# Kernel optimization log

Hardware: AMD Instinct MI355X
Metric: run time of the kernel (lower is better)

## Reference

```python
import jax, jax.numpy as jnp
import numpy as np

SCALE = 0.1
TEMP = 1.0
LN_EPS = 1e-6
NORM_EPS = 1e-12  # torch F.normalize eps

def setup_inputs() -> dict:
    key = jax.random.key(0)
    k1, = jax.random.split(key, 1)
    x = jax.random.normal(k1, (8192, 512), dtype=jnp.float32)
    gamma = jnp.ones((512,), dtype=jnp.float32)
    beta = jnp.zeros((512,), dtype=jnp.float32)
    return {"x": x, "gamma": gamma, "beta": beta}

def reference(x, gamma, beta):
    # L2-normalize rows (torch F.normalize semantics: x / max(||x||, eps))
    norm = jnp.maximum(jnp.linalg.norm(x, axis=1, keepdims=True), NORM_EPS)
    xn = x / norm                                   # [N, d]
    sim = (xn @ xn.T) / TEMP                        # [N, N]
    # dual_norm: row softmax + column softmax
    sim = jax.nn.softmax(sim, axis=1) + jax.nn.softmax(sim, axis=0)
    x_neg = sim @ x                                 # [N, d]
    y = x - SCALE * x_neg
    # LayerNorm over last dim, eps=1e-6
    mean = jnp.mean(y, axis=-1, keepdims=True)
    var = jnp.mean(jnp.square(y - mean), axis=-1, keepdims=True)
    out = (y - mean) * jax.lax.rsqrt(var + LN_EPS) * gamma + beta
    return out
```

## Files before the change

kernel.cpp:

```cpp
#include <hip/hip_runtime.h>
#include <math.h>

#define NN 8192
#define DD 512

constexpr float SCALE_C = 0.1f;
constexpr float LN_EPS_C = 1e-6f;
constexpr float NORM_EPS_C = 1e-12f;
constexpr float CBIG = 32768.0f;
constexpr float INV_CBIG = 1.0f / 32768.0f;

typedef __attribute__((ext_vector_type(8))) short bf16x8;
typedef __attribute__((ext_vector_type(4))) float f32x4;

#define MFMA16(a, b, c) __builtin_amdgcn_mfma_f32_16x16x32_bf16((a), (b), (c), 0, 0, 0)
#define MFMA8(a, b, c)                                                        \
  __builtin_amdgcn_mfma_f32_16x16x32_fp8_fp8((long)(a), (long)(b), (c), 0, 0, 0)

#define GLL16(g, l)                                                        \
  __builtin_amdgcn_global_load_lds(                                        \
      (const __attribute__((address_space(1))) unsigned int*)(g),          \
      (__attribute__((address_space(3))) unsigned int*)(l), 16, 0, 0)

#define WAITV4() asm volatile("s_waitcnt vmcnt(4)" ::: "memory")
#define WAITV0() asm volatile("s_waitcnt vmcnt(0)" ::: "memory")
#define WAITLGKM0() asm volatile("s_waitcnt lgkmcnt(0)" ::: "memory")
#define FENCE() asm volatile("" ::: "memory")
#define BAR() __builtin_amdgcn_s_barrier()

__device__ inline unsigned short f2bf(float f) {
  unsigned int u = __builtin_bit_cast(unsigned int, f);
  unsigned int r = (u + 0x7FFFu + ((u >> 16) & 1u)) >> 16;
  return (unsigned short)r;
}

__device__ inline unsigned int f2fp8n(float f) {
  unsigned int a = __builtin_bit_cast(unsigned int, f);
  unsigned int r = a + 0x7FFFFu + ((a >> 20) & 1u);
  return (r >> 20) - 960u;
}

__device__ inline unsigned int f2fp8(float f) {
  unsigned int u = __builtin_bit_cast(unsigned int, f);
  unsigned int s = (u >> 24) & 0x80u;
  unsigned int a = u & 0x7fffffffu;
  if (a >= 0x3C800000u) {
    unsigned int r = a + 0x7FFFFu + ((a >> 20) & 1u);
    return s | ((r >> 20) - 960u);
  }
  float af = __builtin_bit_cast(float, a);
  return s | (unsigned int)(int)rintf(af * 512.0f);
}

__device__ inline float fp82f(unsigned int b) {
  return __builtin_bit_cast(float, (b + 960u) << 20);
}

__global__ __launch_bounds__(256) void k_prep2(const float* __restrict__ x,
                                               unsigned short* __restrict__ xnb,
                                               unsigned char* __restrict__ xT8) {
  __shared__ unsigned int T8w[16][130];
  const int j0 = blockIdx.x * 16;
  const int t = threadIdx.x;
  const int tr = t >> 4, tc = t & 15;
  const int row = j0 + tr;
  const float* xr = x + (size_t)row * DD;
  float4 v[8];
  float ss = 0.f;
#pragma unroll
  for (int k = 0; k < 8; ++k) {
    v[k] = *(const float4*)(xr + tc * 4 + k * 64);
    ss += v[k].x * v[k].x + v[k].y * v[k].y + v[k].z * v[k].z + v[k].w * v[k].w;
  }
#pragma unroll
  for (int off = 1; off < 16; off <<= 1) ss += __shfl_xor(ss, off);
  const float rn = 1.0f / fmaxf(sqrtf(ss), NORM_EPS_C);
#pragma unroll
  for (int k = 0; k < 8; ++k) {
    ushort4 o;
    o.x = f2bf(v[k].x * rn);
    o.y = f2bf(v[k].y * rn);
    o.z = f2bf(v[k].z * rn);
    o.w = f2bf(v[k].w * rn);
    *(ushort4*)(xnb + (size_t)row * DD + tc * 4 + k * 64) = o;
    T8w[tr][tc + k * 16] = f2fp8(v[k].x) | (f2fp8(v[k].y) << 8) |
                           (f2fp8(v[k].z) << 16) | (f2fp8(v[k].w) << 24);
  }
  __syncthreads();
#pragma unroll
  for (int q = 0; q < 2; ++q) {
    const int d = t + q * 256;
    const unsigned char* col = (const unsigned char*)&T8w[0][0] + d;
    unsigned int wds[4];
#pragma unroll
    for (int p = 0; p < 4; ++p)
      wds[p] = (unsigned int)col[(p * 4 + 0) * 520] |
               ((unsigned int)col[(p * 4 + 1) * 520] << 8) |
               ((unsigned int)col[(p * 4 + 2) * 520] << 16) |
               ((unsigned int)col[(p * 4 + 3) * 520] << 24);
    *(uint4*)&xT8[(size_t)d * NN + j0] = make_uint4(wds[0], wds[1], wds[2], wds[3]);
  }
}

__global__ __launch_bounds__(256, 4) void k_rowsumE(const unsigned short* __restrict__ xnb,
                                                    float* __restrict__ lpart,
                                                    unsigned char* __restrict__ E8) {
  __shared__ __align__(16) unsigned char POOL[32768];
  __shared__ float red[4][64];
  __shared__ float red2[4][64];

  int b = blockIdx.x, bi = 0;
  while (b >= 64 - bi) { b -= 64 - bi; ++bi; }
  const int bj = bi + b;
  const int i0 = bi * 128, j0 = bj * 128;
  const int diag = (bi == bj);

  const int t = threadIdx.x;
  const int w = t >> 6, l = t & 63;
  const int lr = l & 15, lg = l >> 4;
  const int wr = w >> 1, wc = w & 1;
  const int r0 = w * 16 + (l >> 2);
  const int clog = (l & 3) ^ ((r0 >> 1) & 3);
  const unsigned short* gA = xnb + (size_t)(i0 + r0) * DD + clog * 8;
  const unsigned short* gB = xnb + (size_t)(j0 + r0) * DD + clog * 8;

#define RS_STAGE(s, koff)                                                        \
  do {                                                                           \
    GLL16(gA + (koff), (unsigned short*)(POOL + (s) * 16384) + w * 512);         \
    GLL16(gA + (size_t)64 * DD + (koff),                                         \
          (unsigned short*)(POOL + (s) * 16384 + 4096) + w * 512);               \
    GLL16(gB + (koff), (unsigned short*)(POOL + (s) * 16384 + 8192) + w * 512);  \
    GLL16(gB + (size_t)64 * DD + (koff),                                         \
          (unsigned short*)(POOL + (s) * 16384 + 12288) + w * 512);              \
  } while (0)

  RS_STAGE(0, 0);
  RS_STAGE(1, 32);

  f32x4 acc[4][4] = {};
  for (int ks = 0; ks < 16; ++ks) {
    if (ks + 1 < 16) { WAITV4(); } else { WAITV0(); }
    BAR(); FENCE();
    const char* AS = (const char*)(POOL + (ks & 1) * 16384);
    const char* BS = AS + 8192;
    bf16x8 af[4], bv[4];
#pragma unroll
    for (int fm = 0; fm < 4; ++fm) {
      const int row = wr * 64 + fm * 16 + lr;
      af[fm] = *(const bf16x8*)(AS + row * 64 + ((lg ^ ((row >> 1) & 3)) << 4));
    }
#pragma unroll
    for (int fn = 0; fn < 4; ++fn) {
      const int row = wc * 64 + fn * 16 + lr;
      bv[fn] = *(const bf16x8*)(BS + row * 64 + ((lg ^ ((row >> 1) & 3)) << 4));
    }
    WAITLGKM0();
    BAR(); FENCE();
    if (ks + 2 < 16) RS_STAGE(ks & 1, (size_t)(ks + 2) * 32);
#pragma unroll
    for (int fm = 0; fm < 4; ++fm)
#pragma unroll
      for (int fn = 0; fn < 4; ++fn)
        acc[fm][fn] = MFMA16(af[fm], bv[fn], acc[fm][fn]);
  }

  unsigned int ebw[4][4];
  float rsum[4][4] = {};
  float csum[4] = {};
#pragma unroll
  for (int fm = 0; fm < 4; ++fm)
#pragma unroll
    for (int fn = 0; fn < 4; ++fn) {
      unsigned int pw = 0;
#pragma unroll
      for (int rr = 0; rr < 4; ++rr) {
        float e = __expf(acc[fm][fn][rr]);
        rsum[fm][rr] += e;
        csum[fn] += e;
        pw |= f2fp8n(e) << (8 * rr);
      }
      ebw[fm][fn] = pw;
    }

#pragma unroll
  for (int fm = 0; fm < 4; ++fm)
#pragma unroll
    for (int rr = 0; rr < 4; ++rr) {
      float s = rsum[fm][rr];
#pragma unroll
      for (int off = 1; off < 16; off <<= 1) s += __shfl_xor(s, off);
      if (lr == 0) red[w][fm * 16 + lg * 4 + rr] = s;
    }
  if (!diag) {
#pragma unroll
    for (int fn = 0; fn < 4; ++fn) {
      float cs = csum[fn];
      cs += __shfl_xor(cs, 16);
      cs += __shfl_xor(cs, 32);
      if (lg == 0) red2[w][fn * 16 + lr] = cs;
    }
  }

  unsigned char(*Et2)[144] = (unsigned char(*)[144])POOL;
#pragma unroll
  for (int fm = 0; fm < 4; ++fm)
#pragma unroll
    for (int fn = 0; fn < 4; ++fn)
      *(unsigned int*)&Et2[wc * 64 + fn * 16 + lr][wr * 64 + fm * 16 + lg * 4] =
          ebw[fm][fn];
  __syncthreads();
  {
    unsigned char* dst2 = E8 + ((size_t)(bj * 64 + bi) << 14);
#pragma unroll
    for (int q = 0; q < 4; ++q) {
      const int f = t + q * 256;
      *(uint4*)(dst2 + f * 16) = *(const uint4*)&Et2[f >> 3][(f & 7) * 16];
    }
  }
  if (t < 128) {
    const int wrx = t >> 6, idx = t & 63;
    lpart[(size_t)bj * NN + i0 + t] = red[2 * wrx][idx] + red[2 * wrx + 1][idx];
  } else if (!diag) {
    const int c = t - 128;
    const int wcx = c >> 6, idx = c & 63;
    lpart[(size_t)bi * NN + j0 + c] = red2[wcx][idx] + red2[2 + wcx][idx];
  }
}

__global__ __launch_bounds__(256) void k_recip(const float* __restrict__ lpart,
                                               float* __restrict__ rl) {
  const int i = blockIdx.x * 256 + threadIdx.x;
  float s = 0.f;
  for (int c = 0; c < 64; ++c) s += lpart[(size_t)c * NN + i];
  rl[i] = CBIG / s;
}

__global__ __launch_bounds__(256) void k_scale2(unsigned char* __restrict__ P,
                                                const float* __restrict__ rl) {
  __shared__ unsigned int T32[128][35];
  int b = blockIdx.x, ti = 0;
  while (b >= 64 - ti) { b -= 64 - ti; ++ti; }
  const int tj = ti + b;
  const int i0 = ti * 128, j0 = tj * 128;
  const int t = threadIdx.x;
  unsigned char* tileC = P + ((size_t)(tj * 64 + ti) << 14);

#pragma unroll
  for (int q = 0; q < 4; ++q) {
    const int f = t + q * 256;
    const int r = f >> 3;
    const int c0 = (f & 7) * 16;
    uint4 v = *(const uint4*)(tileC + f * 16);
    const float rlr = rl[j0 + r];
    float rlc[16];
#pragma unroll
    for (int p = 0; p < 4; ++p) {
      float4 r4 = *(const float4*)(rl + i0 + c0 + p * 4);
      rlc[p * 4 + 0] = r4.x; rlc[p * 4 + 1] = r4.y;
      rlc[p * 4 + 2] = r4.z; rlc[p * 4 + 3] = r4.w;
    }
    unsigned int wsrc[4] = {v.x, v.y, v.z, v.w};
    unsigned int wdst[4];
#pragma unroll
    for (int p = 0; p < 4; ++p) {
      unsigned int in = wsrc[p], out = 0;
#pragma unroll
      for (int k = 0; k < 4; ++k) {
        float e = fp82f((in >> (8 * k)) & 0xffu);
        out |= f2fp8n(e * (rlr + rlc[p * 4 + k])) << (8 * k);
      }
      wdst[p] = out;
      T32[r][(c0 >> 2) + p] = out;
    }
    *(uint4*)(tileC + f * 16) = make_uint4(wdst[0], wdst[1], wdst[2], wdst[3]);
  }
  if (ti == tj) return;
  __syncthreads();

  unsigned char* tileT = P + ((size_t)(ti * 64 + tj) << 14);
  {
    const int rg = t >> 3;
    const int cc = t & 7;
    const int c2 = cc * 16;
    unsigned int o[4][4];
#pragma unroll
    for (int k4 = 0; k4 < 4; ++k4) {
      unsigned int a0 = T32[c2 + k4 * 4 + 0][rg];
      unsigned int a1 = T32[c2 + k4 * 4 + 1][rg];
      unsigned int a2 = T32[c2 + k4 * 4 + 2][rg];
      unsigned int a3 = T32[c2 + k4 * 4 + 3][rg];
      unsigned int b0 = (a0 & 0x00FF00FFu) | ((a1 << 8) & 0xFF00FF00u);
      unsigned int b1 = ((a0 >> 8) & 0x00FF00FFu) | (a1 & 0xFF00FF00u);
      unsigned int b2 = (a2 & 0x00FF00FFu) | ((a3 << 8) & 0xFF00FF00u);
      unsigned int b3 = ((a2 >> 8) & 0x00FF00FFu) | (a3 & 0xFF00FF00u);
      o[0][k4] = (b0 & 0x0000FFFFu) | (b2 << 16);
      o[1][k4] = (b1 & 0x0000FFFFu) | (b3 << 16);
      o[2][k4] = (b0 >> 16) | (b2 & 0xFFFF0000u);
      o[3][k4] = (b1 >> 16) | (b3 & 0xFFFF0000u);
    }
#pragma unroll
    for (int i = 0; i < 4; ++i)
      *(uint4*)(tileT + (size_t)(rg * 4 + i) * 128 + c2) =
          make_uint4(o[i][0], o[i][1], o[i][2], o[i][3]);
  }
}

__global__ __launch_bounds__(256, 4) void k_pv3(const unsigned char* __restrict__ P8,
                                                const unsigned char* __restrict__ xT8,
                                                unsigned short* __restrict__ parts) {
  __shared__ __align__(16) unsigned char POOL[34816];
  const int i0 = blockIdx.x * 128;
  const int n0 = blockIdx.y * 128;
  const int z = blockIdx.z;
  const int t = threadIdx.x;
  const int w = t >> 6, l = t & 63;
  const int lr = l & 15, lg = l >> 4;
  const int wr = w >> 1, wc = w & 1;
  const int r0 = w * 16 + (l >> 2);
  const int clog = (l & 3) ^ ((r0 >> 1) & 3);
  const unsigned char* Abase = P8 + ((size_t)((i0 >> 7) * 64 + z * 16) << 14) +
                               r0 * 128 + clog * 16;
  const unsigned char* gB = xT8 + (size_t)(n0 + r0) * NN + z * 2048 + clog * 16;

#define PV_STAGE(s, koff)                                                      \
  do {                                                                         \
    const unsigned char* a_ = Abase + (((koff) >> 7) << 14) + ((koff) & 127);  \
    GLL16(a_, POOL + (s) * 8192 + w * 1024);                                   \
    GLL16(a_ + 8192, POOL + (s) * 8192 + 4096 + w * 1024);                     \
    GLL16(gB + (koff), POOL + 16384 + (s) * 8192 + w * 1024);                  \
    GLL16(gB + (size_t)64 * NN + (koff),                                       \
          POOL + 16384 + (s) * 8192 + 4096 + w * 1024);                        \
  } while (0)

  PV_STAGE(0, 0);
  PV_STAGE(1, 64);

  f32x4 acc[4][4] = {};
  for (int ks = 0; ks < 32; ++ks) {
    if (ks + 1 < 32) { WAITV4(); } else { WAITV0(); }
    BAR(); FENCE();
    const char* AS = (const char*)(POOL + (ks & 1) * 8192);
    const char* BS = (const char*)(POOL + 16384 + (ks & 1) * 8192);
    unsigned long long af[4][2], bv[4][2];
#pragma unroll
    for (int fm = 0; fm < 4; ++fm) {
      const int row = wr * 64 + fm * 16 + lr;
      const int swz = (row >> 1) & 3;
#pragma unroll
      for (int kk = 0; kk < 2; ++kk) {
        int off = row * 64 + (((kk * 2 + (lg >> 1)) ^ swz) << 4) + ((lg & 1) << 3);
        af[fm][kk] = *(const unsigned long long*)(AS + off);
      }
    }
#pragma unroll
    for (int fn = 0; fn < 4; ++fn) {
      const int row = wc * 64 + fn * 16 + lr;
      const int swz = (row >> 1) & 3;
#pragma unroll
      for (int kk = 0; kk < 2; ++kk) {
        int off = row * 64 + (((kk * 2 + (lg >> 1)) ^ swz) << 4) + ((lg & 1) << 3);
        bv[fn][kk] = *(const unsigned long long*)(BS + off);
      }
    }
    WAITLGKM0();
    BAR(); FENCE();
    if (ks + 2 < 32) PV_STAGE(ks & 1, (ks + 2) * 64);
#pragma unroll
    for (int kk = 0; kk < 2; ++kk)
#pragma unroll
      for (int fm = 0; fm < 4; ++fm)
#pragma unroll
        for (int fn = 0; fn < 4; ++fn)
          acc[fm][fn] = MFMA8(af[fm][kk], bv[fn][kk], acc[fm][fn]);
  }

  BAR(); FENCE();
  unsigned short* Pt = (unsigned short*)POOL;
#pragma unroll
  for (int fm = 0; fm < 4; ++fm)
#pragma unroll
    for (int fn = 0; fn < 4; ++fn) {
      const int col = wc * 64 + fn * 16 + lr;
#pragma unroll
      for (int rr = 0; rr < 4; ++rr) {
        const int row = wr * 64 + fm * 16 + lg * 4 + rr;
        Pt[row * 136 + col] = f2bf(acc[fm][fn][rr] * INV_CBIG);
      }
    }
  __syncthreads();
  {
    unsigned short* dst = parts + (size_t)z * NN * DD + (size_t)i0 * DD + n0;
#pragma unroll
    for (int q = 0; q < 8; ++q) {
      const int f = t + q * 256;
      const int row = f >> 4, ch = f & 15;
      *(uint4*)(dst + (size_t)row * DD + ch * 8) =
          *(const uint4*)&Pt[row * 136 + ch * 8];
    }
  }
}

__global__ __launch_bounds__(128) void k_ln(const float* __restrict__ x,
                                            float* __restrict__ out,
                                            const unsigned short* __restrict__ parts,
                                            const float* __restrict__ gamma,
                                            const float* __restrict__ beta) {
  const int row = blockIdx.x;
  const int t = threadIdx.x;
  float4 p = make_float4(0.f, 0.f, 0.f, 0.f);
#pragma unroll
  for (int s = 0; s < 4; ++s) {
    ushort4 q = ((const ushort4*)(parts + (size_t)s * NN * DD + (size_t)row * DD))[t];
    p.x += __builtin_bit_cast(float, (unsigned int)q.x << 16);
    p.y += __builtin_bit_cast(float, (unsigned int)q.y << 16);
    p.z += __builtin_bit_cast(float, (unsigned int)q.z << 16);
    p.w += __builtin_bit_cast(float, (unsigned int)q.w << 16);
  }
  float4 xv = ((const float4*)(x + (size_t)row * DD))[t];
  float4 y;
  y.x = xv.x - SCALE_C * p.x;
  y.y = xv.y - SCALE_C * p.y;
  y.z = xv.z - SCALE_C * p.z;
  y.w = xv.w - SCALE_C * p.w;
  float sum = y.x + y.y + y.z + y.w;
#pragma unroll
  for (int off = 32; off; off >>= 1) sum += __shfl_down(sum, off);
  __shared__ float ra[2], rb[2];
  if ((t & 63) == 0) ra[t >> 6] = sum;
  __syncthreads();
  float mean = (ra[0] + ra[1]) * (1.0f / DD);
  float d0 = y.x - mean, d1 = y.y - mean, d2 = y.z - mean, d3 = y.w - mean;
  float vs = d0 * d0 + d1 * d1 + d2 * d2 + d3 * d3;
#pragma unroll
  for (int off = 32; off; off >>= 1) vs += __shfl_down(vs, off);
  if ((t & 63) == 0) rb[t >> 6] = vs;
  __syncthreads();
  float rstd = rsqrtf((rb[0] + rb[1]) * (1.0f / DD) + LN_EPS_C);
  float4 g4 = ((const float4*)gamma)[t];
  float4 b4 = ((const float4*)beta)[t];
  float4 o;
  o.x = d0 * rstd * g4.x + b4.x;
  o.y = d1 * rstd * g4.y + b4.y;
  o.z = d2 * rstd * g4.z + b4.z;
  o.w = d3 * rstd * g4.w + b4.w;
  ((float4*)(out + (size_t)row * DD))[t] = o;
}

extern "C" void kernel_launch(void* const* d_in, const int* in_sizes, int n_in,
                              void* d_out, int out_size, void* d_ws, size_t ws_size,
                              hipStream_t stream) {
  const float* x = (const float*)d_in[0];
  const float* gamma = (const float*)d_in[1];
  const float* beta = (const float*)d_in[2];
  float* out = (float*)d_out;

  unsigned short* xnb = (unsigned short*)d_ws;
  unsigned char* xT8 = (unsigned char*)(xnb + (size_t)NN * DD);
  float* lpart = (float*)(xT8 + (size_t)NN * DD);
  float* rl = lpart + (size_t)64 * NN;
  unsigned short* parts = (unsigned short*)(rl + NN);
  unsigned char* E8 = (unsigned char*)(parts + (size_t)4 * NN * DD);

  k_prep2<<<NN / 16, 256, 0, stream>>>(x, xnb, xT8);
  k_rowsumE<<<2080, 256, 0, stream>>>(xnb, lpart, E8);
  k_recip<<<NN / 256, 256, 0, stream>>>(lpart, rl);
  k_scale2<<<2080, 256, 0, stream>>>(E8, rl);
  k_pv3<<<dim3(64, 4, 4), 256, 0, stream>>>(E8, xT8, parts);
  k_ln<<<NN, 128, 0, stream>>>(x, out, parts, gamma, beta);
}
```

Baseline: 148.1 us.

## Restructure rowsumE GEMM pipeline with 64-wide K tiles and double-buffered LDS

Reworks the k_rowsumE bf16 GEMM main loop. K tiles grow to 64 elements, each split into two 32-wide sub-stages, and LDS grows to 64KB so a whole next tile can be prefetched while the current one is consumed. This drops the second barrier per step, which cuts barrier count, and MFMA issue priority is raised with s_setprio. In exchange LDS use doubles and launch bounds fall from 4 to 2 blocks per CU, which reduces occupancy.

Result: slower. 165.1 us (+11.4%).

```diff
diff --git a/kernel.cpp b/kernel.cpp
--- a/kernel.cpp
+++ b/kernel.cpp
@@ -102,10 +102,10 @@
   }
 }
 
-__global__ __launch_bounds__(256, 4) void k_rowsumE(const unsigned short* __restrict__ xnb,
+__global__ __launch_bounds__(256, 2) void k_rowsumE(const unsigned short* __restrict__ xnb,
                                                     float* __restrict__ lpart,
                                                     unsigned char* __restrict__ E8) {
-  __shared__ __align__(16) unsigned char POOL[32768];
+  __shared__ __align__(16) unsigned char POOL[65536];
   __shared__ float red[4][64];
   __shared__ float red2[4][64];
 
@@ -119,50 +119,57 @@
   const int w = t >> 6, l = t & 63;
   const int lr = l & 15, lg = l >> 4;
   const int wr = w >> 1, wc = w & 1;
-  const int r0 = w * 16 + (l >> 2);
-  const int clog = (l & 3) ^ ((r0 >> 1) & 3);
-  const unsigned short* gA = xnb + (size_t)(i0 + r0) * DD + clog * 8;
-  const unsigned short* gB = xnb + (size_t)(j0 + r0) * DD + clog * 8;
-
-#define RS_STAGE(s, koff)                                                        \
-  do {                                                                           \
-    GLL16(gA + (koff), (unsigned short*)(POOL + (s) * 16384) + w * 512);         \
-    GLL16(gA + (size_t)64 * DD + (koff),                                         \
-          (unsigned short*)(POOL + (s) * 16384 + 4096) + w * 512);               \
-    GLL16(gB + (koff), (unsigned short*)(POOL + (s) * 16384 + 8192) + w * 512);  \
-    GLL16(gB + (size_t)64 * DD + (koff),                                         \
-          (unsigned short*)(POOL + (s) * 16384 + 12288) + w * 512);              \
+
+#define RS2_STAGE(bufb, kt, s)                                                 \
+  do {                                                                        \
+    _Pragma("unroll") for (int q_ = 0; q_ < 2; ++q_) {                        \
+      const int f_ = w * 128 + q_ * 64 + l;                                   \
+      const int row_ = f_ >> 2, c2_ = f_ & 3;                                 \
+      const size_t ko_ =                                                      \
+          (size_t)(kt) * 64 + (s) * 32 + ((c2_ ^ ((row_ >> 1) & 3)) * 8);     \
+      GLL16(xnb + (size_t)(i0 + row_) * DD + ko_,                             \
+            POOL + (bufb) * 32768 + (s) * 8192 + w * 2048 + q_ * 1024);       \
+      GLL16(xnb + (size_t)(j0 + row_) * DD + ko_,                             \
+            POOL + (bufb) * 32768 + 16384 + (s) * 8192 + w * 2048 + q_ * 1024); \
+    }                                                                         \
   } while (0)
 
-  RS_STAGE(0, 0);
-  RS_STAGE(1, 32);
+  RS2_STAGE(0, 0, 0);
+  RS2_STAGE(0, 0, 1);
 
   f32x4 acc[4][4] = {};
-  for (int ks = 0; ks < 16; ++ks) {
-    if (ks + 1 < 16) { WAITV4(); } else { WAITV0(); }
-    BAR(); FENCE();
-    const char* AS = (const char*)(POOL + (ks & 1) * 16384);
-    const char* BS = AS + 8192;
-    bf16x8 af[4], bv[4];
-#pragma unroll
-    for (int fm = 0; fm < 4; ++fm) {
-      const int row = wr * 64 + fm * 16 + lr;
-      af[fm] = *(const bf16x8*)(AS + row * 64 + ((lg ^ ((row >> 1) & 3)) << 4));
-    }
-#pragma unroll
-    for (int fn = 0; fn < 4; ++fn) {
-      const int row = wc * 64 + fn * 16 + lr;
-      bv[fn] = *(const bf16x8*)(BS + row * 64 + ((lg ^ ((row >> 1) & 3)) << 4));
-    }
-    WAITLGKM0();
-    BAR(); FENCE();
-    if (ks + 2 < 16) RS_STAGE(ks & 1, (size_t)(ks + 2) * 32);
-#pragma unroll
-    for (int fm = 0; fm < 4; ++fm)
-#pragma unroll
-      for (int fn = 0; fn < 4; ++fn)
-        acc[fm][fn] = MFMA16(af[fm], bv[fn], acc[fm][fn]);
-  }
+  for (int kt = 0; kt < 8; ++kt) {
+    const int buf = kt & 1;
+    const char* Ab = (const char*)(POOL + buf * 32768);
+    const char* Bb = Ab + 16384;
+#pragma unroll
+    for (int s = 0; s < 2; ++s) {
+      if (kt + 1 < 8 || s == 0) { WAITV4(); } else { WAITV0(); }
+      BAR(); FENCE();
+      if (kt + 1 < 8) RS2_STAGE(buf ^ 1, kt + 1, s);
+      bf16x8 af[4], bv[4];
+#pragma unroll
+      for (int fm = 0; fm < 4; ++fm) {
+        const int row = wr * 64 + fm * 16 + lr;
+        af[fm] = *(const bf16x8*)(Ab + s * 8192 + row * 64 +
+                                  ((lg ^ ((row >> 1) & 3)) << 4));
+      }
+#pragma unroll
+      for (int fn = 0; fn < 4; ++fn) {
+        const int row = wc * 64 + fn * 16 + lr;
+        bv[fn] = *(const bf16x8*)(Bb + s * 8192 + row * 64 +
+                                  ((lg ^ ((row >> 1) & 3)) << 4));
+      }
+      __builtin_amdgcn_s_setprio(1);
+#pragma unroll
+      for (int fm = 0; fm < 4; ++fm)
+#pragma unroll
+        for (int fn = 0; fn < 4; ++fn)
+          acc[fm][fn] = MFMA16(af[fm], bv[fn], acc[fm][fn]);
+      __builtin_amdgcn_s_setprio(0);
+    }
+  }
+  BAR(); FENCE();
 
   unsigned int ebw[4][4];
   float rsum[4][4] = {};
```
